# Kernel optimization log

Measured on AMD Instinct MI355X. Metric: run time of the kernel, lower is better.

Reference implementation:

```python
import jax, jax.numpy as jnp
import numpy as np

N = 100000
E = 600000
F_IN = 128
HID = 256
C = 64


def setup_inputs() -> dict:
    key = jax.random.key(0)
    ks = jax.random.split(key, 6)
    x = jax.random.normal(ks[0], (N, F_IN), dtype=jnp.float32)
    edge_index = jax.random.randint(ks[1], (2, E), 0, N, dtype=jnp.int64)
    W1 = jax.random.normal(ks[2], (F_IN, HID), dtype=jnp.float32) * (1.0 / np.sqrt(F_IN))
    b1 = jnp.zeros((HID,), dtype=jnp.float32)
    W2 = jax.random.normal(ks[3], (HID, C), dtype=jnp.float32) * (1.0 / np.sqrt(HID))
    b2 = jnp.zeros((C,), dtype=jnp.float32)
    return {"x": x, "W1": W1, "b1": b1, "W2": W2, "b2": b2, "edge_index": edge_index}


def _gcn_conv(h, W, b, src, dst, norm, self_w):
    # h: [N, F_in] -> [N, F_out]; symmetric-normalized aggregation over A+I
    h = h @ W  # [N, F_out]
    agg = jax.ops.segment_sum(h[src] * norm[:, None], dst, num_segments=N)
    agg = agg + h * self_w[:, None]  # self-loop contribution d^{-1/2}*d^{-1/2}
    return agg + b


def reference(x, W1, b1, W2, b2, edge_index):
    src, dst = edge_index[0], edge_index[1]
    # degree of A + I (self-loops added): 1 + in-degree
    deg = jnp.ones((N,), dtype=x.dtype).at[dst].add(1.0)
    dinv = jax.lax.rsqrt(deg)
    norm = dinv[src] * dinv[dst]  # [E]
    self_w = dinv * dinv          # [N]

    h = _gcn_conv(x, W1, b1, src, dst, norm, self_w)
    h = jax.nn.relu(h)
    # dropout is identity in eval mode (training=False)
    out = _gcn_conv(h, W2, b2, src, dst, norm, self_w)
    return jax.nn.log_softmax(out, axis=1)
```

## Files before the change

### kernel.cpp

```cpp
#include <hip/hip_runtime.h>
#include <cstdint>
#include <cstddef>

#define N_NODES 100000
#define N_EDGES 600000
#define F_IN    128
#define HID     256
#define NC      64
#define NB_SCAN 391

typedef __attribute__((ext_vector_type(8))) short bf16x8;
typedef __attribute__((ext_vector_type(4))) float f32x4;

__device__ __forceinline__ unsigned short f2bf(float f) {
    unsigned int u = __float_as_uint(f);
    u = (u + 0x7FFFu + ((u >> 16) & 1u)) >> 16;
    return (unsigned short)u;
}
__device__ __forceinline__ float bf2f(unsigned short u) {
    return __uint_as_float(((unsigned int)u) << 16);
}

__global__ void k_detect(const int* __restrict__ ei_words, int* __restrict__ mode) {
    if (blockIdx.x == 0 && threadIdx.x == 0) {
        int allz = 1;
        for (int i = 0; i < 64; ++i) {
            long long s = (long long)i * (N_EDGES - 1) / 63;
            if (ei_words[2 * s + 1] != 0) { allz = 0; break; }
        }
        *mode = allz;
    }
}

__device__ __forceinline__ int load_idx(const void* ei, int m, long long i) {
    return m ? (int)((const long long*)ei)[i] : ((const int*)ei)[i];
}

__global__ void k_zero(int* __restrict__ p, int n) {
    int i = blockIdx.x * blockDim.x + threadIdx.x;
    if (i < n) p[i] = 0;
}

__global__ void k_hist(const void* __restrict__ ei, const int* __restrict__ mode,
                       int* __restrict__ deg) {
    int e = blockIdx.x * blockDim.x + threadIdx.x;
    if (e >= N_EDGES) return;
    int d = load_idx(ei, *mode, (long long)N_EDGES + e);
    atomicAdd(&deg[d], 1);
}

__global__ void k_scanA(const int* __restrict__ deg, int* __restrict__ ptmp,
                        int* __restrict__ bsum) {
    __shared__ int sm[256];
    int i = blockIdx.x * 256 + threadIdx.x;
    int v = (i < N_NODES) ? deg[i] : 0;
    sm[threadIdx.x] = v;
    __syncthreads();
    for (int off = 1; off < 256; off <<= 1) {
        int t = (threadIdx.x >= off) ? sm[threadIdx.x - off] : 0;
        __syncthreads();
        sm[threadIdx.x] += t;
        __syncthreads();
    }
    if (i < N_NODES) ptmp[i] = sm[threadIdx.x] - v;
    if (threadIdx.x == 255) bsum[blockIdx.x] = sm[255];
}

__global__ void k_scanB(int* __restrict__ bsum) {
    __shared__ int sm[512];
    int i = threadIdx.x;
    int v = (i < NB_SCAN) ? bsum[i] : 0;
    sm[i] = v;
    __syncthreads();
    for (int off = 1; off < 512; off <<= 1) {
        int t = (i >= off) ? sm[i - off] : 0;
        __syncthreads();
        sm[i] += t;
        __syncthreads();
    }
    if (i < NB_SCAN) bsum[i] = sm[i] - v;
}

__global__ void k_scanC(const int* __restrict__ deg, const int* __restrict__ ptmp,
                        const int* __restrict__ bsum, int* __restrict__ row_ptr,
                        int* __restrict__ cursor, float* __restrict__ dinv) {
    int i = blockIdx.x * 256 + threadIdx.x;
    if (i < N_NODES) {
        int rp = ptmp[i] + bsum[blockIdx.x];
        row_ptr[i] = rp;
        cursor[i]  = rp;
        dinv[i]    = rsqrtf(1.0f + (float)deg[i]);
    }
    if (i == 0) row_ptr[N_NODES] = N_EDGES;
}

__global__ void k_fill(const void* __restrict__ ei, const int* __restrict__ mode,
                       int* __restrict__ cursor, int* __restrict__ csr_src) {
    int e = blockIdx.x * blockDim.x + threadIdx.x;
    if (e >= N_EDGES) return;
    int m = *mode;
    int s = load_idx(ei, m, e);
    int d = load_idx(ei, m, (long long)N_EDGES + e);
    int pos = atomicAdd(&cursor[d], 1);
    csr_src[pos] = s;
}

#define XB_BLOCKS (N_NODES * F_IN / 8 / 256)
#define W1_BLOCKS (F_IN * HID / 256)
#define W2_BLOCKS (HID * NC / 256)
__global__ void k_prep(const float* __restrict__ x, const float* __restrict__ W1,
                       const float* __restrict__ W2, unsigned short* __restrict__ xbf,
                       unsigned short* __restrict__ W1T, unsigned short* __restrict__ W2T) {
    int bid = blockIdx.x;
    int tid = threadIdx.x;
    if (bid < XB_BLOCKS) {
        int i = bid * 256 + tid;
        const float4* xr = (const float4*)x;
        float4 a = xr[(size_t)i * 2];
        float4 b = xr[(size_t)i * 2 + 1];
        bf16x8 o;
        o[0] = (short)f2bf(a.x); o[1] = (short)f2bf(a.y);
        o[2] = (short)f2bf(a.z); o[3] = (short)f2bf(a.w);
        o[4] = (short)f2bf(b.x); o[5] = (short)f2bf(b.y);
        o[6] = (short)f2bf(b.z); o[7] = (short)f2bf(b.w);
        *(bf16x8*)(xbf + (size_t)i * 8) = o;
    } else if (bid < XB_BLOCKS + W1_BLOCKS) {
        int i = (bid - XB_BLOCKS) * 256 + tid;
        int k = i >> 8, n = i & 255;
        W1T[n * F_IN + k] = f2bf(W1[i]);
    } else {
        int i = (bid - XB_BLOCKS - W1_BLOCKS) * 256 + tid;
        int k = i >> 6, n = i & 63;
        W2T[n * HID + k] = f2bf(W2[i]);
    }
}

__global__ void k_gather1(const unsigned short* __restrict__ xbf,
                          const int* __restrict__ row_ptr,
                          const int* __restrict__ csr_src, const float* __restrict__ dinv,
                          unsigned short* __restrict__ px) {
    int g = threadIdx.x >> 4;
    int j = threadIdx.x & 15;
    int n = blockIdx.x * 16 + g;
    float dn = dinv[n];
    bf16x8 sv = *(const bf16x8*)(xbf + (size_t)n * F_IN + j * 8);
    float acc[8];
#pragma unroll
    for (int t = 0; t < 8; ++t) acc[t] = bf2f((unsigned short)sv[t]) * dn;
    int e0 = row_ptr[n], e1 = row_ptr[n + 1];
    for (int k = e0; k < e1; ++k) {
        int s = csr_src[k];
        float w = dinv[s];
        bf16x8 v = *(const bf16x8*)(xbf + (size_t)s * F_IN + j * 8);
#pragma unroll
        for (int t = 0; t < 8; ++t)
            acc[t] = fmaf(bf2f((unsigned short)v[t]), w, acc[t]);
    }
    bf16x8 o;
#pragma unroll
    for (int t = 0; t < 8; ++t) o[t] = (short)f2bf(acc[t] * dn);
    *(bf16x8*)(px + (size_t)n * F_IN + j * 8) = o;
}

__global__ __launch_bounds__(256, 4) void k_mlp_fused(
        const unsigned short* __restrict__ px, const unsigned short* __restrict__ W1T,
        const float* __restrict__ b1, const unsigned short* __restrict__ W2T,
        unsigned short* __restrict__ hx2) {
    __shared__ unsigned short hlds[32 * HID];
    const int lane = threadIdx.x & 63;
    const int w    = threadIdx.x >> 6;
    const int l15  = lane & 15, lhi = lane >> 4;
    const int row0 = blockIdx.x * 32;

    {
        const int col0 = w * 64;
        bf16x8 a[4][2];
#pragma unroll
        for (int ks = 0; ks < 4; ++ks)
#pragma unroll
            for (int mt = 0; mt < 2; ++mt)
                a[ks][mt] = *(const bf16x8*)(px + (size_t)(row0 + mt * 16 + l15) * F_IN + ks * 32 + lhi * 8);

        f32x4 acc[2][4];
#pragma unroll
        for (int mt = 0; mt < 2; ++mt)
#pragma unroll
            for (int nt = 0; nt < 4; ++nt) acc[mt][nt] = (f32x4){0.f, 0.f, 0.f, 0.f};

#pragma unroll
        for (int ks = 0; ks < 4; ++ks) {
#pragma unroll
            for (int nt = 0; nt < 4; ++nt) {
                bf16x8 b = *(const bf16x8*)(W1T + (size_t)(col0 + nt * 16 + l15) * F_IN + ks * 32 + lhi * 8);
#pragma unroll
                for (int mt = 0; mt < 2; ++mt)
                    acc[mt][nt] = __builtin_amdgcn_mfma_f32_16x16x32_bf16(b, a[ks][mt], acc[mt][nt], 0, 0, 0);
            }
        }

#pragma unroll
        for (int mt = 0; mt < 2; ++mt) {
            const int lr = mt * 16 + l15;
#pragma unroll
            for (int nt = 0; nt < 4; ++nt) {
                int c0 = col0 + nt * 16 + lhi * 4;
                float4 bb = *(const float4*)(b1 + c0);
                ushort4 o;
                o.x = f2bf(fmaxf(acc[mt][nt][0] + bb.x, 0.f));
                o.y = f2bf(fmaxf(acc[mt][nt][1] + bb.y, 0.f));
                o.z = f2bf(fmaxf(acc[mt][nt][2] + bb.z, 0.f));
                o.w = f2bf(fmaxf(acc[mt][nt][3] + bb.w, 0.f));
                unsigned byte = (unsigned)(lr * (HID * 2) + c0 * 2) ^ ((lr & 7) << 4);
                *(ushort4*)((char*)hlds + byte) = o;
            }
        }
    }
    __syncthreads();

    {
        const int lr = (w & 1) * 16 + l15;
        const int cb = (w >> 1) * 32;
        bf16x8 a2[8];
#pragma unroll
        for (int ks = 0; ks < 8; ++ks) {
            unsigned byte = (unsigned)(lr * (HID * 2) + ks * 64 + lhi * 16) ^ ((lr & 7) << 4);
            a2[ks] = *(const bf16x8*)((const char*)hlds + byte);
        }
        f32x4 acc2[2];
#pragma unroll
        for (int nt = 0; nt < 2; ++nt) acc2[nt] = (f32x4){0.f, 0.f, 0.f, 0.f};
#pragma unroll
        for (int nt = 0; nt < 2; ++nt) {
            const unsigned short* pb = W2T + (size_t)(cb + nt * 16 + l15) * HID + lhi * 8;
#pragma unroll
            for (int ks = 0; ks < 8; ++ks) {
                bf16x8 b = *(const bf16x8*)(pb + ks * 32);
                acc2[nt] = __builtin_amdgcn_mfma_f32_16x16x32_bf16(b, a2[ks], acc2[nt], 0, 0, 0);
            }
        }
        const int r = row0 + lr;
#pragma unroll
        for (int nt = 0; nt < 2; ++nt) {
            int c0 = cb + nt * 16 + lhi * 4;
            ushort4 o;
            o.x = f2bf(acc2[nt][0]); o.y = f2bf(acc2[nt][1]);
            o.z = f2bf(acc2[nt][2]); o.w = f2bf(acc2[nt][3]);
            *(ushort4*)(hx2 + (size_t)r * NC + c0) = o;
        }
    }
}

__global__ void k_gather2sm(const unsigned short* __restrict__ hx2,
                            const int* __restrict__ row_ptr,
                            const int* __restrict__ csr_src, const float* __restrict__ dinv,
                            const float* __restrict__ b2, float* __restrict__ out) {
    int g = threadIdx.x >> 4;
    int j = threadIdx.x & 15;
    int n = blockIdx.x * 16 + g;
    float dn = dinv[n];
    ushort4 sv = *(const ushort4*)(hx2 + (size_t)n * NC + j * 4);
    float ax = bf2f(sv.x) * dn, ay = bf2f(sv.y) * dn,
          az = bf2f(sv.z) * dn, aw = bf2f(sv.w) * dn;
    int e0 = row_ptr[n], e1 = row_ptr[n + 1];
    for (int k = e0; k < e1; ++k) {
        int s = csr_src[k];
        float wv = dinv[s];
        ushort4 v = *(const ushort4*)(hx2 + (size_t)s * NC + j * 4);
        ax = fmaf(bf2f(v.x), wv, ax); ay = fmaf(bf2f(v.y), wv, ay);
        az = fmaf(bf2f(v.z), wv, az); aw = fmaf(bf2f(v.w), wv, aw);
    }
    const float4 b = ((const float4*)b2)[j];
    float4 o;
    o.x = fmaf(ax, dn, b.x); o.y = fmaf(ay, dn, b.y);
    o.z = fmaf(az, dn, b.z); o.w = fmaf(aw, dn, b.w);
    float mx = fmaxf(fmaxf(o.x, o.y), fmaxf(o.z, o.w));
#pragma unroll
    for (int msk = 8; msk; msk >>= 1) mx = fmaxf(mx, __shfl_xor(mx, msk));
    float s4 = expf(o.x - mx) + expf(o.y - mx) + expf(o.z - mx) + expf(o.w - mx);
#pragma unroll
    for (int msk = 8; msk; msk >>= 1) s4 += __shfl_xor(s4, msk);
    float ls = mx + logf(s4);
    o.x -= ls; o.y -= ls; o.z -= ls; o.w -= ls;
    ((float4*)out)[(size_t)n * 16 + j] = o;
}

extern "C" void kernel_launch(void* const* d_in, const int* in_sizes, int n_in,
                              void* d_out, int out_size, void* d_ws, size_t ws_size,
                              hipStream_t stream) {
    const float* x  = (const float*)d_in[0];
    const float* W1 = (const float*)d_in[1];
    const float* b1 = (const float*)d_in[2];
    const float* W2 = (const float*)d_in[3];
    const float* b2 = (const float*)d_in[4];
    const void*  ei = d_in[5];
    float* out = (float*)d_out;

    char* ws = (char*)d_ws;
    size_t off = 0;
    auto alloc = [&](size_t bytes) {
        char* p = ws + off;
        off += (bytes + 255) & ~(size_t)255;
        return p;
    };
    int*            mode    = (int*)            alloc(4);
    int*            deg     = (int*)            alloc((size_t)N_NODES * 4);
    int*            ptmp    = (int*)            alloc((size_t)N_NODES * 4);
    int*            bsum    = (int*)            alloc(4096);
    int*            row_ptr = (int*)            alloc((size_t)(N_NODES + 1) * 4);
    int*            cursor  = (int*)            alloc((size_t)N_NODES * 4);
    float*          dinv    = (float*)          alloc((size_t)N_NODES * 4);
    int*            csr_src = (int*)            alloc((size_t)N_EDGES * 4);
    unsigned short* W1T     = (unsigned short*) alloc((size_t)F_IN * HID * 2);
    unsigned short* W2T     = (unsigned short*) alloc((size_t)HID * NC * 2);
    unsigned short* xbf     = (unsigned short*) alloc((size_t)N_NODES * F_IN * 2);
    unsigned short* px      = (unsigned short*) alloc((size_t)(N_NODES + 64) * F_IN * 2);
    unsigned short* hx2     = (unsigned short*) alloc((size_t)(N_NODES + 64) * NC * 2);

    k_detect<<<1, 64, 0, stream>>>((const int*)ei, mode);

    k_zero<<<(N_NODES + 255) / 256, 256, 0, stream>>>(deg, N_NODES);
    k_hist<<<(N_EDGES + 255) / 256, 256, 0, stream>>>(ei, mode, deg);
    k_scanA<<<NB_SCAN, 256, 0, stream>>>(deg, ptmp, bsum);
    k_scanB<<<1, 512, 0, stream>>>(bsum);
    k_scanC<<<NB_SCAN, 256, 0, stream>>>(deg, ptmp, bsum, row_ptr, cursor, dinv);
    k_fill<<<(N_EDGES + 255) / 256, 256, 0, stream>>>(ei, mode, cursor, csr_src);

    k_prep<<<XB_BLOCKS + W1_BLOCKS + W2_BLOCKS, 256, 0, stream>>>(x, W1, W2, xbf, W1T, W2T);

    k_gather1<<<N_NODES / 16, 256, 0, stream>>>(xbf, row_ptr, csr_src, dinv, px);
    k_mlp_fused<<<N_NODES / 32, 256, 0, stream>>>(px, W1T, b1, W2T, hx2);
    k_gather2sm<<<N_NODES / 16, 256, 0, stream>>>(hx2, row_ptr, csr_src, dinv, b2, out);
}
```

Before: 221.2 us.

## Fuse layer-1 neighbor gather into MLP kernel via swizzled LDS staging

Removes the separate first-layer gather kernel. The fused MLP kernel now aggregates each of its 32 rows' neighbor features into a swizzled LDS tile, using 8 threads per row with 16 features each, and reads its MFMA A-operands from LDS. This drops one launch and the global write and re-read of the px intermediate. In exchange, the gather now has less parallelism per node, the kernel uses more LDS, and the launch_bounds occupancy hint is gone, so register pressure and occupancy may change.

```diff
diff --git a/kernel.cpp b/kernel.cpp
--- a/kernel.cpp
+++ b/kernel.cpp
@@ -135,37 +135,12 @@
     }
 }
 
-__global__ void k_gather1(const unsigned short* __restrict__ xbf,
-                          const int* __restrict__ row_ptr,
-                          const int* __restrict__ csr_src, const float* __restrict__ dinv,
-                          unsigned short* __restrict__ px) {
-    int g = threadIdx.x >> 4;
-    int j = threadIdx.x & 15;
-    int n = blockIdx.x * 16 + g;
-    float dn = dinv[n];
-    bf16x8 sv = *(const bf16x8*)(xbf + (size_t)n * F_IN + j * 8);
-    float acc[8];
-#pragma unroll
-    for (int t = 0; t < 8; ++t) acc[t] = bf2f((unsigned short)sv[t]) * dn;
-    int e0 = row_ptr[n], e1 = row_ptr[n + 1];
-    for (int k = e0; k < e1; ++k) {
-        int s = csr_src[k];
-        float w = dinv[s];
-        bf16x8 v = *(const bf16x8*)(xbf + (size_t)s * F_IN + j * 8);
-#pragma unroll
-        for (int t = 0; t < 8; ++t)
-            acc[t] = fmaf(bf2f((unsigned short)v[t]), w, acc[t]);
-    }
-    bf16x8 o;
-#pragma unroll
-    for (int t = 0; t < 8; ++t) o[t] = (short)f2bf(acc[t] * dn);
-    *(bf16x8*)(px + (size_t)n * F_IN + j * 8) = o;
-}
-
-__global__ __launch_bounds__(256, 4) void k_mlp_fused(
-        const unsigned short* __restrict__ px, const unsigned short* __restrict__ W1T,
-        const float* __restrict__ b1, const unsigned short* __restrict__ W2T,
-        unsigned short* __restrict__ hx2) {
+__global__ __launch_bounds__(256) void k_mlp_fused(
+        const unsigned short* __restrict__ xbf, const int* __restrict__ row_ptr,
+        const int* __restrict__ csr_src, const float* __restrict__ dinv,
+        const unsigned short* __restrict__ W1T, const float* __restrict__ b1,
+        const unsigned short* __restrict__ W2T, unsigned short* __restrict__ hx2) {
+    __shared__ unsigned short px_lds[32 * F_IN];
     __shared__ unsigned short hlds[32 * HID];
     const int lane = threadIdx.x & 63;
     const int w    = threadIdx.x >> 6;
@@ -173,13 +148,56 @@
     const int row0 = blockIdx.x * 32;
 
     {
+        const int r   = threadIdx.x >> 3;
+        const int seg = threadIdx.x & 7;
+        const int n   = row0 + r;
+        const float dn = dinv[n];
+        float acc16[16];
+        const unsigned short* xp = xbf + (size_t)n * F_IN + seg * 16;
+        bf16x8 v0 = *(const bf16x8*)(xp);
+        bf16x8 v1 = *(const bf16x8*)(xp + 8);
+#pragma unroll
+        for (int t = 0; t < 8; ++t) {
+            acc16[t]     = bf2f((unsigned short)v0[t]) * dn;
+            acc16[8 + t] = bf2f((unsigned short)v1[t]) * dn;
+        }
+        int e0 = row_ptr[n], e1 = row_ptr[n + 1];
+        for (int k = e0; k < e1; ++k) {
+            int s = csr_src[k];
+            float wv = dinv[s];
+            const unsigned short* sp = xbf + (size_t)s * F_IN + seg * 16;
+            bf16x8 u0 = *(const bf16x8*)(sp);
+            bf16x8 u1 = *(const bf16x8*)(sp + 8);
+#pragma unroll
+            for (int t = 0; t < 8; ++t) {
+                acc16[t]     = fmaf(bf2f((unsigned short)u0[t]), wv, acc16[t]);
+                acc16[8 + t] = fmaf(bf2f((unsigned short)u1[t]), wv, acc16[8 + t]);
+            }
+        }
+        bf16x8 w0, w1;
+#pragma unroll
+        for (int t = 0; t < 8; ++t) {
+            w0[t] = (short)f2bf(acc16[t] * dn);
+            w1[t] = (short)f2bf(acc16[8 + t] * dn);
+        }
+        unsigned base = (unsigned)(r * 256 + seg * 32);
+        unsigned sw   = (unsigned)((r & 7) << 4);
+        *(bf16x8*)((char*)px_lds + ((base) ^ sw))      = w0;
+        *(bf16x8*)((char*)px_lds + ((base + 16) ^ sw)) = w1;
+    }
+    __syncthreads();
+
+    {
         const int col0 = w * 64;
         bf16x8 a[4][2];
 #pragma unroll
         for (int ks = 0; ks < 4; ++ks)
 #pragma unroll
-            for (int mt = 0; mt < 2; ++mt)
-                a[ks][mt] = *(const bf16x8*)(px + (size_t)(row0 + mt * 16 + l15) * F_IN + ks * 32 + lhi * 8);
+            for (int mt = 0; mt < 2; ++mt) {
+                unsigned byte = (unsigned)((mt * 16 + l15) * 256 + ks * 64 + lhi * 16)
+                              ^ (unsigned)((l15 & 7) << 4);
+                a[ks][mt] = *(const bf16x8*)((const char*)px_lds + byte);
+            }
 
         f32x4 acc[2][4];
 #pragma unroll
@@ -313,7 +331,6 @@
     unsigned short* W1T     = (unsigned short*) alloc((size_t)F_IN * HID * 2);
     unsigned short* W2T     = (unsigned short*) alloc((size_t)HID * NC * 2);
     unsigned short* xbf     = (unsigned short*) alloc((size_t)N_NODES * F_IN * 2);
-    unsigned short* px      = (unsigned short*) alloc((size_t)(N_NODES + 64) * F_IN * 2);
     unsigned short* hx2     = (unsigned short*) alloc((size_t)(N_NODES + 64) * NC * 2);
 
     k_detect<<<1, 64, 0, stream>>>((const int*)ei, mode);
@@ -327,7 +344,7 @@
 
     k_prep<<<XB_BLOCKS + W1_BLOCKS + W2_BLOCKS, 256, 0, stream>>>(x, W1, W2, xbf, W1T, W2T);
 
-    k_gather1<<<N_NODES / 16, 256, 0, stream>>>(xbf, row_ptr, csr_src, dinv, px);
-    k_mlp_fused<<<N_NODES / 32, 256, 0, stream>>>(px, W1T, b1, W2T, hx2);
+    k_mlp_fused<<<N_NODES / 32, 256, 0, stream>>>(xbf, row_ptr, csr_src, dinv,
+                                                  W1T, b1, W2T, hx2);
     k_gather2sm<<<N_NODES / 16, 256, 0, stream>>>(hx2, row_ptr, csr_src, dinv, b2, out);
 }
```

Measured after the change: 200.2 us. -9.5%, faster.
